# Performance work log

Measured on AMD Instinct MI355X. Metric: run time of the kernel, lower is better.

## Reference

```python
import jax, jax.numpy as jnp
import numpy as np

DIM = 256; HEADS = 4; HD = DIM // HEADS; SCALE = HD ** -0.5
CBS = 4; CSTRIDE = 2; SBS = 4; NSEL = 16; WS = 7
B = 4; H = 64; W = 64


def _unfold(x, bs, stride):
    # x: (B,H,W,C) -> (B, nh*nw, C*bs*bs), flat channel order matches torch F.unfold
    # (index = c*bs*bs + kh*bs + kw)
    b, h, w, c = x.shape
    nh = (h - bs) // stride + 1
    nw = (w - bs) // stride + 1
    cols = [x[:, kh:kh + nh * stride:stride, kw:kw + nw * stride:stride, :]
            for kh in range(bs) for kw in range(bs)]
    p = jnp.stack(cols, axis=-1)  # (B,nh,nw,C,bs*bs)
    return p.reshape(b, nh * nw, c * bs * bs)


def _rel_pos_index(ws):
    coords = np.stack(np.meshgrid(np.arange(ws), np.arange(ws), indexing='ij')).reshape(2, -1)
    rel = (coords[:, :, None] - coords[:, None, :]).transpose(1, 2, 0).copy()
    rel[:, :, 0] += ws - 1
    rel[:, :, 1] += ws - 1
    rel[:, :, 0] *= 2 * ws - 1
    return jnp.asarray(rel.sum(-1))  # (ws*ws, ws*ws) int


def _mlp(x, w1, b1, w2, b2):
    return jax.nn.gelu(x @ w1 + b1, approximate=False) @ w2 + b2


def _window_attn(x, qkv_w, qkv_b, proj_w, proj_b, bias_table):
    b, c, h, w = x.shape
    ws = WS
    ph = (ws - h % ws) % ws
    pw = (ws - w % ws) % ws
    xp = jnp.pad(x, ((0, 0), (0, 0), (0, ph), (0, pw)))
    hp, wp = h + ph, w + pw
    xw = xp.reshape(b, c, hp // ws, ws, wp // ws, ws).transpose(0, 2, 4, 3, 5, 1).reshape(-1, ws * ws, c)
    bw = xw.shape[0]
    qkv = (xw @ qkv_w + qkv_b).reshape(bw, ws * ws, 3, HEADS, HD).transpose(2, 0, 3, 1, 4)
    q, k, v = qkv[0], qkv[1], qkv[2]
    attn = jnp.einsum('bhnd,bhmd->bhnm', q, k) * SCALE
    rpi = _rel_pos_index(ws)
    bias = bias_table[rpi.reshape(-1)].reshape(ws * ws, ws * ws, HEADS).transpose(2, 0, 1)
    attn = jax.nn.softmax(attn + bias[None], axis=-1)
    o = jnp.einsum('bhnm,bhmd->bhnd', attn, v).transpose(0, 2, 1, 3).reshape(bw, ws * ws, c)
    o = o @ proj_w + proj_b
    o = o.reshape(b, hp // ws, wp // ws, ws, ws, c).transpose(0, 5, 1, 3, 2, 4).reshape(b, c, hp, wp)
    return o[:, :, :h, :w]


def _forward(x, qkv_cmp_w, qkv_cmp_b, qkv_slc_w, qkv_slc_b,
             cmpk_w1, cmpk_b1, cmpk_w2, cmpk_b2,
             cmpv_w1, cmpv_b1, cmpv_w2, cmpv_b2, pos_embed,
             win_qkv_w, win_qkv_b, win_proj_w, win_proj_b, win_bias_table,
             proj_cmp_w, proj_cmp_b, proj_slc_w, proj_slc_b,
             gate_w1, gate_b1, gate_w2, gate_b2):
    b, c, h, w = x.shape
    n = h * w
    xs = x.reshape(b, c, n).transpose(0, 2, 1)  # (B,N,C)

    # --- compressed branch ---
    qkv = (xs @ qkv_cmp_w + qkv_cmp_b).reshape(b, n, 3, HEADS, HD).transpose(2, 0, 3, 1, 4)
    q_c, k_c, v_c = qkv[0], qkv[1], qkv[2]  # (B,heads,N,hd)
    k_flat = k_c.transpose(0, 2, 1, 3).reshape(b, n, c)
    v_flat = v_c.transpose(0, 2, 1, 3).reshape(b, n, c)
    fk = _unfold(k_flat.reshape(b, h, w, c), CBS, CSTRIDE)  # (B,nb,C*16)
    fv = _unfold(v_flat.reshape(b, h, w, c), CBS, CSTRIDE)
    nb = fk.shape[1]
    # replicate torch's reshape of the channel-major unfold vector into (bs*bs, dim)
    kpos = (fk.reshape(b, nb, CBS * CBS, c) + pos_embed[None]).reshape(b, nb, CBS * CBS * c)
    k_cmp = _mlp(kpos, cmpk_w1, cmpk_b1, cmpk_w2, cmpk_b2)  # (B,nb,C)
    v_cmp = _mlp(fv, cmpv_w1, cmpv_b1, cmpv_w2, cmpv_b2)
    kch = k_cmp.reshape(b, nb, HEADS, HD).transpose(0, 2, 1, 3)
    vch = v_cmp.reshape(b, nb, HEADS, HD).transpose(0, 2, 1, 3)
    attn_cmp = jax.nn.softmax(jnp.einsum('bhnd,bhmd->bhnm', q_c, kch) * SCALE, axis=-1)
    out_cmp = jnp.einsum('bhnm,bhmd->bhnd', attn_cmp, vch).transpose(0, 2, 1, 3).reshape(b, n, c)
    out_cmp = out_cmp @ proj_cmp_w + proj_cmp_b

    # --- selected branch ---
    qkv2 = (xs @ qkv_slc_w + qkv_slc_b).reshape(b, n, 3, HEADS, HD).transpose(2, 0, 3, 1, 4)
    q_s, k_s, v_s = qkv2[0], qkv2[1], qkv2[2]
    ks_flat = k_s.transpose(0, 2, 1, 3).reshape(b, n, c)
    vs_flat = v_s.transpose(0, 2, 1, 3).reshape(b, n, c)
    imp = attn_cmp.sum(axis=1).mean(axis=1)  # (B, nb)
    ns = min(NSEL, nb)
    _, idx = jax.lax.top_k(imp, ns)
    fkb = _unfold(ks_flat.reshape(b, h, w, c), SBS, SBS)
    fvb = _unfold(vs_flat.reshape(b, h, w, c), SBS, SBS)
    nb2 = fkb.shape[1]
    kb = fkb.reshape(b, nb2, SBS * SBS, c)
    vb = fvb.reshape(b, nb2, SBS * SBS, c)
    idx = jnp.clip(idx, 0, nb2 - 1)
    k_slc = jnp.take_along_axis(kb, idx[:, :, None, None], axis=1).reshape(b, ns * SBS * SBS, c)
    v_slc = jnp.take_along_axis(vb, idx[:, :, None, None], axis=1).reshape(b, ns * SBS * SBS, c)
    ksh = k_slc.reshape(b, -1, HEADS, HD).transpose(0, 2, 1, 3)
    vsh = v_slc.reshape(b, -1, HEADS, HD).transpose(0, 2, 1, 3)
    attn_slc = jax.nn.softmax(jnp.einsum('bhnd,bhmd->bhnm', q_s, ksh) * SCALE, axis=-1)
    out_slc = jnp.einsum('bhnm,bhmd->bhnd', attn_slc, vsh).transpose(0, 2, 1, 3).reshape(b, n, c)
    out_slc = out_slc @ proj_slc_w + proj_slc_b

    # --- window branch ---
    out_win = _window_attn(x, win_qkv_w, win_qkv_b, win_proj_w, win_proj_b, win_bias_table)
    out_win = out_win.reshape(b, c, n).transpose(0, 2, 1)

    # --- gated combination ---
    g = jax.nn.sigmoid(jax.nn.gelu(xs @ gate_w1 + gate_b1, approximate=False) @ gate_w2 + gate_b2)
    out = g[..., 0:1] * out_cmp + g[..., 1:2] * out_slc + g[..., 2:3] * out_win
    return out.transpose(0, 2, 1).reshape(b, c, h, w)


def setup_inputs() -> dict:
    key = jax.random.key(0)
    ks = jax.random.split(key, 16)
    s = 0.02
    d = {
        'x': jax.random.normal(ks[0], (B, DIM, H, W), jnp.float32),
        'qkv_cmp_w': jax.random.normal(ks[1], (DIM, 3 * DIM)) * s,
        'qkv_cmp_b': jnp.zeros((3 * DIM,)),
        'qkv_slc_w': jax.random.normal(ks[2], (DIM, 3 * DIM)) * s,
        'qkv_slc_b': jnp.zeros((3 * DIM,)),
        'cmpk_w1': jax.random.normal(ks[3], (DIM * CBS * CBS, 2 * DIM)) * s,
        'cmpk_b1': jnp.zeros((2 * DIM,)),
        'cmpk_w2': jax.random.normal(ks[4], (2 * DIM, DIM)) * s,
        'cmpk_b2': jnp.zeros((DIM,)),
        'cmpv_w1': jax.random.normal(ks[5], (DIM * CBS * CBS, 2 * DIM)) * s,
        'cmpv_b1': jnp.zeros((2 * DIM,)),
        'cmpv_w2': jax.random.normal(ks[6], (2 * DIM, DIM)) * s,
        'cmpv_b2': jnp.zeros((DIM,)),
        'pos_embed': jax.random.normal(ks[7], (1, CBS * CBS, DIM)) * s,
        'win_qkv_w': jax.random.normal(ks[8], (DIM, 3 * DIM)) * s,
        'win_qkv_b': jnp.zeros((3 * DIM,)),
        'win_proj_w': jax.random.normal(ks[9], (DIM, DIM)) * s,
        'win_proj_b': jnp.zeros((DIM,)),
        'win_bias_table': jax.random.normal(ks[10], ((2 * WS - 1) ** 2, HEADS)) * s,
        'proj_cmp_w': jax.random.normal(ks[11], (DIM, DIM)) * s,
        'proj_cmp_b': jnp.zeros((DIM,)),
        'proj_slc_w': jax.random.normal(ks[12], (DIM, DIM)) * s,
        'proj_slc_b': jnp.zeros((DIM,)),
        'gate_w1': jax.random.normal(ks[13], (DIM, DIM // 4)) * s,
        'gate_b1': jnp.zeros((DIM // 4,)),
        'gate_w2': jax.random.normal(ks[14], (DIM // 4, 3)) * s,
        'gate_b2': jnp.zeros((3,)),
    }
    return d


def reference(x, qkv_cmp_w, qkv_cmp_b, qkv_slc_w, qkv_slc_b,
              cmpk_w1, cmpk_b1, cmpk_w2, cmpk_b2,
              cmpv_w1, cmpv_b1, cmpv_w2, cmpv_b2, pos_embed,
              win_qkv_w, win_qkv_b, win_proj_w, win_proj_b, win_bias_table,
              proj_cmp_w, proj_cmp_b, proj_slc_w, proj_slc_b,
              gate_w1, gate_b1, gate_w2, gate_b2):
    return _forward(x, qkv_cmp_w, qkv_cmp_b, qkv_slc_w, qkv_slc_b,
                    cmpk_w1, cmpk_b1, cmpk_w2, cmpk_b2,
                    cmpv_w1, cmpv_b1, cmpv_w2, cmpv_b2, pos_embed,
                    win_qkv_w, win_qkv_b, win_proj_w, win_proj_b, win_bias_table,
                    proj_cmp_w, proj_cmp_b, proj_slc_w, proj_slc_b,
                    gate_w1, gate_b1, gate_w2, gate_b2)
```

## Files before the change

kernel.cpp:

```cpp
#include <hip/hip_runtime.h>
#include <stdint.h>
#include <stddef.h>


#define DEV __device__ __forceinline__

typedef __attribute__((ext_vector_type(8))) short short8;
typedef __attribute__((ext_vector_type(4))) float f32x4;
typedef unsigned short u16;

DEV u16 f2bf(float f){
    unsigned u = __float_as_uint(f);
    u += 0x7FFFu + ((u>>16)&1u);
    return (u16)(u>>16);
}
DEV float bf2f(u16 u){ return __uint_as_float(((unsigned)u)<<16); }

__global__ void k_xs(const float* __restrict__ x, u16* __restrict__ xh,
                     u16* __restrict__ xl){
    __shared__ float t[32][33];
    int b = blockIdx.z; int c0 = blockIdx.y*32; int n0 = blockIdx.x*32;
    int tx = threadIdx.x, ty = threadIdx.y;
    for(int i=ty;i<32;i+=8)
        t[i][tx] = x[((size_t)(b*256 + c0+i))*4096 + n0 + tx];
    __syncthreads();
    for(int i=ty;i<32;i+=8){
        float v = t[tx][i];
        u16 h = f2bf(v);
        size_t o = ((size_t)(b*4096 + n0+i))*256 + c0 + tx;
        xh[o] = h;
        xl[o] = f2bf(v - bf2f(h));
    }
}

__global__ void k_wt(const float* __restrict__ W, u16* __restrict__ WT,
                     int K, int N){
    __shared__ float t[32][33];
    int k0 = blockIdx.x*32, n0 = blockIdx.y*32;
    int tx = threadIdx.x, ty = threadIdx.y;
    for(int i=ty;i<32;i+=8)
        if(k0+i<K && n0+tx<N) t[i][tx] = W[(size_t)(k0+i)*N + n0+tx];
    __syncthreads();
    for(int i=ty;i<32;i+=8)
        if(n0+i<N && k0+tx<K) WT[(size_t)(n0+i)*K + k0+tx] = f2bf(t[tx][i]);
}

__global__ void k_wt2(const float* __restrict__ W, u16* __restrict__ Hi,
                      u16* __restrict__ Lo, int K, int N){
    __shared__ float t[32][33];
    int k0 = blockIdx.x*32, n0 = blockIdx.y*32;
    int tx = threadIdx.x, ty = threadIdx.y;
    for(int i=ty;i<32;i+=8)
        if(k0+i<K && n0+tx<N) t[i][tx] = W[(size_t)(k0+i)*N + n0+tx];
    __syncthreads();
    for(int i=ty;i<32;i+=8)
        if(n0+i<N && k0+tx<K){
            float v = t[tx][i];
            u16 h = f2bf(v);
            Hi[(size_t)(n0+i)*K + k0+tx] = h;
            Lo[(size_t)(n0+i)*K + k0+tx] = f2bf(v - bf2f(h));
        }
}

__global__ void k_vt(const float* __restrict__ vc, u16* __restrict__ vt,
                     int NK, int ldk){
    __shared__ float t[32][33];
    int b = blockIdx.z; int k0 = blockIdx.x*32; int c0 = blockIdx.y*32;
    int tx = threadIdx.x, ty = threadIdx.y;
    for(int i=ty;i<32;i+=8){
        int k = k0+i;
        t[i][tx] = (k < NK) ? vc[((size_t)(b*NK + k))*256 + c0 + tx] : 0.f;
    }
    __syncthreads();
    for(int i=ty;i<32;i+=8){
        int k = k0+tx;
        if(k < ldk)
            vt[((size_t)(b*256 + c0+i))*ldk + k] = f2bf(t[tx][i]);
    }
}

__global__ __launch_bounds__(256) void k_gemm(
        const float* __restrict__ A, const float* __restrict__ W,
        const float* __restrict__ bias, float* __restrict__ C,
        int M, int K, int Nn, int act)
{
    __shared__ float As[16][68];
    __shared__ float Bs[16][64];
    const int m0 = blockIdx.y*64, n0 = blockIdx.x*64;
    const int t = threadIdx.x, tx = t&15, ty = t>>4;
    float acc[4][4] = {};
    const int am = t>>2;
    const int ak = (t&3)*4;
    const bool arow_ok = (m0+am) < M;

    for(int k0=0;k0<K;k0+=16){
        float4 av = make_float4(0.f,0.f,0.f,0.f);
        if(arow_ok) av = *reinterpret_cast<const float4*>(&A[(size_t)(m0+am)*K + k0 + ak]);
        As[ak+0][am]=av.x; As[ak+1][am]=av.y; As[ak+2][am]=av.z; As[ak+3][am]=av.w;
        {
            int n = t&63, kb = t>>6;
            #pragma unroll
            for(int r=0;r<4;r++){
                int kk = r*4 + kb; float v = 0.f;
                if(n0+n < Nn) v = W[(size_t)(k0+kk)*Nn + n0+n];
                Bs[kk][n] = v;
            }
        }
        __syncthreads();
        #pragma unroll
        for(int kk=0;kk<16;kk++){
            float a0=As[kk][ty*4+0], a1=As[kk][ty*4+1], a2=As[kk][ty*4+2], a3=As[kk][ty*4+3];
            float b0=Bs[kk][tx*4+0], b1=Bs[kk][tx*4+1], b2=Bs[kk][tx*4+2], b3=Bs[kk][tx*4+3];
            acc[0][0]=fmaf(a0,b0,acc[0][0]); acc[0][1]=fmaf(a0,b1,acc[0][1]);
            acc[0][2]=fmaf(a0,b2,acc[0][2]); acc[0][3]=fmaf(a0,b3,acc[0][3]);
            acc[1][0]=fmaf(a1,b0,acc[1][0]); acc[1][1]=fmaf(a1,b1,acc[1][1]);
            acc[1][2]=fmaf(a1,b2,acc[1][2]); acc[1][3]=fmaf(a1,b3,acc[1][3]);
            acc[2][0]=fmaf(a2,b0,acc[2][0]); acc[2][1]=fmaf(a2,b1,acc[2][1]);
            acc[2][2]=fmaf(a2,b2,acc[2][2]); acc[2][3]=fmaf(a2,b3,acc[2][3]);
            acc[3][0]=fmaf(a3,b0,acc[3][0]); acc[3][1]=fmaf(a3,b1,acc[3][1]);
            acc[3][2]=fmaf(a3,b2,acc[3][2]); acc[3][3]=fmaf(a3,b3,acc[3][3]);
        }
        __syncthreads();
    }
    #pragma unroll
    for(int i=0;i<4;i++){
        int m = m0 + ty*4 + i;
        if(m >= M) continue;
        #pragma unroll
        for(int j=0;j<4;j++){
            int n = n0 + tx*4 + j;
            if(n >= Nn) continue;
            float v = acc[i][j] + (bias ? bias[n] : 0.f);
            if(act==1)      v = 0.5f*v*(1.0f + erff(v*0.70710678118654752f));
            else if(act==2) v = 1.0f/(1.0f + expf(-v));
            C[(size_t)m*Nn + n] = v;
        }
    }
}

template<int WM, int WN, int AM, int BMD, int NSPLIT, int OBF>
__global__ __launch_bounds__(256) void k_mgs(
        const float* __restrict__ Af, const u16* __restrict__ Ah,
        const u16* __restrict__ Al,
        const float* __restrict__ Bf, const u16* __restrict__ Bh,
        const u16* __restrict__ Bl,
        const float* __restrict__ bias, float* __restrict__ C,
        u16* __restrict__ Cb, u16* __restrict__ Cb2,
        int M, int N, int K, int lda, int ldb, int ldc, int act, float scale,
        long zsA, long zsB, long zsC)
{
    constexpr int BM = 32*WM, BN = 32*WN;
    constexpr bool SP = (NSPLIT == 3);
    const long zo = (long)blockIdx.z;
    if(AM==0){ Af += zo*zsA; } else { Ah += zo*zsA; if(AM==2) Al += zo*zsA; }
    if(BMD==0){ Bf += zo*zsB; } else { Bh += zo*zsB; if(BMD==2) Bl += zo*zsB; }
    if(OBF) Cb += zo*zsC; else C += zo*zsC;

    __shared__ u16 Ahi[BM*64];
    __shared__ u16 Alo[SP ? BM*64 : 8];
    __shared__ u16 Bhi[BN*64];
    __shared__ u16 Blo[SP ? BN*64 : 8];

    const int m0 = blockIdx.y*BM, n0 = blockIdx.x*BN;
    const int tid = threadIdx.x, lane = tid&63, wv = tid>>6;
    const int wm = (wv>>1)*(16*WM), wn = (wv&1)*(16*WN);
    f32x4 acc[WM][WN] = {};

    constexpr int TPR_A = 256/BM;
    constexpr int CH_A  = 8/TPR_A;
    const int arow = tid / TPR_A;
    const int acol0 = (tid % TPR_A)*(128/TPR_A);
    constexpr int TPR_B = 256/BN;
    constexpr int CH_B  = 8/TPR_B;
    const int brow = tid / TPR_B;
    const int bcol0 = (tid % TPR_B)*(128/TPR_B);

    for(int kt=0; kt<K; kt+=64){
        {
            const bool ok = (m0+arow) < M;
            #pragma unroll
            for(int c=0;c<CH_A;c++){
                int colbyte = acol0 + c*16;
                int e = colbyte>>1;
                const bool lok = ok && (kt + e + 8 <= K);
                short8 h = {}, l = {};
                if(AM==0){
                    float4 v0 = make_float4(0,0,0,0), v1 = v0;
                    if(lok){
                        const float* src = &Af[(size_t)(m0+arow)*lda + kt + e];
                        v0 = *reinterpret_cast<const float4*>(src);
                        v1 = *reinterpret_cast<const float4*>(src+4);
                    }
                    float vv[8] = {v0.x,v0.y,v0.z,v0.w,v1.x,v1.y,v1.z,v1.w};
                    #pragma unroll
                    for(int j=0;j<8;j++){
                        u16 hb = f2bf(vv[j]);
                        h[j] = (short)hb;
                        if(SP) l[j] = (short)f2bf(vv[j] - bf2f(hb));
                    }
                } else {
                    if(lok){
                        h = *reinterpret_cast<const short8*>(Ah + (size_t)(m0+arow)*lda + kt + e);
                        if(SP && AM==2)
                            l = *reinterpret_cast<const short8*>(Al + (size_t)(m0+arow)*lda + kt + e);
                    }
                }
                int byteoff = arow*128 + (colbyte ^ ((arow&7)<<4));
                *reinterpret_cast<short8*>(reinterpret_cast<char*>(Ahi)+byteoff) = h;
                if(SP)
                    *reinterpret_cast<short8*>(reinterpret_cast<char*>(Alo)+byteoff) = l;
            }
        }
        {
            const bool ok = (n0+brow) < N;
            #pragma unroll
            for(int c=0;c<CH_B;c++){
                int colbyte = bcol0 + c*16;
                int e = colbyte>>1;
                const bool lok = ok && (kt + e + 8 <= K);
                short8 h = {}, l = {};
                if(BMD==0){
                    float4 v0 = make_float4(0,0,0,0), v1 = v0;
                    if(lok){
                        const float* src = &Bf[(size_t)(n0+brow)*ldb + kt + e];
                        v0 = *reinterpret_cast<const float4*>(src);
                        v1 = *reinterpret_cast<const float4*>(src+4);
                    }
                    float vv[8] = {v0.x,v0.y,v0.z,v0.w,v1.x,v1.y,v1.z,v1.w};
                    #pragma unroll
                    for(int j=0;j<8;j++){
                        u16 hb = f2bf(vv[j]);
                        h[j] = (short)hb;
                        if(SP) l[j] = (short)f2bf(vv[j] - bf2f(hb));
                    }
                } else {
                    if(lok){
                        h = *reinterpret_cast<const short8*>(Bh + (size_t)(n0+brow)*ldb + kt + e);
                        if(SP && BMD==2)
                            l = *reinterpret_cast<const short8*>(Bl + (size_t)(n0+brow)*ldb + kt + e);
                    }
                }
                int byteoff = brow*128 + (colbyte ^ ((brow&7)<<4));
                *reinterpret_cast<short8*>(reinterpret_cast<char*>(Bhi)+byteoff) = h;
                if(SP)
                    *reinterpret_cast<short8*>(reinterpret_cast<char*>(Blo)+byteoff) = l;
            }
        }
        __syncthreads();
        #pragma unroll
        for(int kb=0;kb<2;kb++){
            short8 ah[WM], al[WM], bh[WN], bl[WN];
            #pragma unroll
            for(int i=0;i<WM;i++){
                int ar = wm + i*16 + (lane&15);
                int ab = ar*128 + (((kb*64) + ((lane>>4)*16)) ^ ((ar&7)<<4));
                ah[i] = *reinterpret_cast<const short8*>(reinterpret_cast<const char*>(Ahi)+ab);
                if(SP)
                    al[i] = *reinterpret_cast<const short8*>(reinterpret_cast<const char*>(Alo)+ab);
            }
            #pragma unroll
            for(int i=0;i<WN;i++){
                int br = wn + i*16 + (lane&15);
                int bb = br*128 + (((kb*64) + ((lane>>4)*16)) ^ ((br&7)<<4));
                bh[i] = *reinterpret_cast<const short8*>(reinterpret_cast<const char*>(Bhi)+bb);
                if(SP)
                    bl[i] = *reinterpret_cast<const short8*>(reinterpret_cast<const char*>(Blo)+bb);
            }
            #pragma unroll
            for(int mi=0;mi<WM;mi++)
                #pragma unroll
                for(int ni=0;ni<WN;ni++){
                    if(SP){
                        acc[mi][ni] = __builtin_amdgcn_mfma_f32_16x16x32_bf16(
                                          al[mi], bh[ni], acc[mi][ni], 0, 0, 0);
                        acc[mi][ni] = __builtin_amdgcn_mfma_f32_16x16x32_bf16(
                                          ah[mi], bl[ni], acc[mi][ni], 0, 0, 0);
                    }
                    acc[mi][ni] = __builtin_amdgcn_mfma_f32_16x16x32_bf16(
                                      ah[mi], bh[ni], acc[mi][ni], 0, 0, 0);
                }
        }
        __syncthreads();
    }
    #pragma unroll
    for(int mi=0;mi<WM;mi++){
        #pragma unroll
        for(int ni=0;ni<WN;ni++){
            int col = n0 + wn + ni*16 + (lane&15);
            if(col >= N) continue;
            int rowb = m0 + wm + mi*16 + ((lane>>4)*4);
            float bv = bias ? bias[col] : 0.f;
            #pragma unroll
            for(int r=0;r<4;r++){
                int m = rowb + r;
                if(m >= M) continue;
                float v = acc[mi][ni][r]*scale + bv;
                if(act==1)      v = 0.5f*v*(1.0f + erff(v*0.70710678118654752f));
                else if(act==2) v = 1.0f/(1.0f + expf(-v));
                if(OBF==2){
                    u16 hb = f2bf(v);
                    Cb [(size_t)m*ldc + col] = hb;
                    Cb2[(size_t)m*ldc + col] = f2bf(v - bf2f(hb));
                } else if(OBF==1){
                    Cb[(size_t)m*ldc + col] = f2bf(v);
                } else {
                    C [(size_t)m*ldc + col] = v;
                }
            }
        }
    }
}

template<int SPLIT, int IMP, int NKR, int NT, int LDV>
__global__ __launch_bounds__(256) void k_fattn(
    const float* __restrict__ Qg, const u16* __restrict__ Khg,
    const u16* __restrict__ Klg, const u16* __restrict__ VTg,
    float* __restrict__ Og, float* __restrict__ impp)
{
    const int qb = blockIdx.x, h = blockIdx.y, b = blockIdx.z;
    const int tid = threadIdx.x, lane = tid&63, wv = tid>>6;
    const int wm = wv*16;
    const int rgrp = lane>>4;
    const int cidx = lane&15;

    __shared__ u16 Qh[64*64];
    __shared__ u16 Ql[SPLIT?64*64:8];
    __shared__ u16 Kh[64*64];
    __shared__ u16 Kl[SPLIT?64*64:8];
    __shared__ u16 Pl[64*64];
    __shared__ u16 Vl[64*64];
    __shared__ float part[4][64];
    __shared__ float colacc[IMP? NT*64 : 8];

    {
        int row = tid>>2;
        int col0 = (tid&3)*32;
        const float* src = &Qg[((size_t)b*4096 + qb*64 + row)*768 + h*64];
        #pragma unroll
        for(int c=0;c<2;c++){
            int colbyte = col0 + c*16;
            int e = colbyte>>1;
            float4 v0 = *reinterpret_cast<const float4*>(src+e);
            float4 v1 = *reinterpret_cast<const float4*>(src+e+4);
            float vv[8]={v0.x,v0.y,v0.z,v0.w,v1.x,v1.y,v1.z,v1.w};
            short8 hh, ll;
            #pragma unroll
            for(int j=0;j<8;j++){
                u16 hb=f2bf(vv[j]); hh[j]=(short)hb;
                if(SPLIT) ll[j]=(short)f2bf(vv[j]-bf2f(hb));
            }
            int byteoff = row*128 + (colbyte ^ ((row&7)<<4));
            *reinterpret_cast<short8*>(reinterpret_cast<char*>(Qh)+byteoff)=hh;
            if(SPLIT)
                *reinterpret_cast<short8*>(reinterpret_cast<char*>(Ql)+byteoff)=ll;
        }
        if(IMP) for(int k=tid;k<NT*64;k+=256) colacc[k]=0.f;
    }

    float m[4], l[4];
    #pragma unroll
    for(int r=0;r<4;r++){ m[r]=-1e30f; l[r]=0.f; }

    for(int t=0;t<NT;t++){
        const int kt = t*64;
        __syncthreads();
        {
            int row = tid>>2;
            int col0 = (tid&3)*32;
            const bool ok = (kt+row) < NKR;
            const u16* srch = &Khg[((size_t)b*NKR + kt + row)*256 + h*64];
            const u16* srcl = SPLIT ? &Klg[((size_t)b*NKR + kt + row)*256 + h*64] : nullptr;
            #pragma unroll
            for(int c=0;c<2;c++){
                int colbyte = col0 + c*16;
                int e = colbyte>>1;
                short8 hh={}, ll={};
                if(ok){
                    hh = *reinterpret_cast<const short8*>(srch+e);
                    if(SPLIT) ll = *reinterpret_cast<const short8*>(srcl+e);
                }
                int byteoff = row*128 + (colbyte ^ ((row&7)<<4));
                *reinterpret_cast<short8*>(reinterpret_cast<char*>(Kh)+byteoff)=hh;
                if(SPLIT)
                    *reinterpret_cast<short8*>(reinterpret_cast<char*>(Kl)+byteoff)=ll;
            }
        }
        __syncthreads();
        f32x4 acc[4] = {};
        #pragma unroll
        for(int kb=0;kb<2;kb++){
            int koff = kb*64 + rgrp*16;
            int ar = wm + cidx;
            int ab = ar*128 + (koff ^ ((ar&7)<<4));
            short8 ah = *reinterpret_cast<const short8*>(reinterpret_cast<const char*>(Qh)+ab);
            short8 al;
            if(SPLIT) al = *reinterpret_cast<const short8*>(reinterpret_cast<const char*>(Ql)+ab);
            #pragma unroll
            for(int ni=0;ni<4;ni++){
                int br = ni*16 + cidx;
                int bb = br*128 + (koff ^ ((br&7)<<4));
                short8 bh = *reinterpret_cast<const short8*>(reinterpret_cast<const char*>(Kh)+bb);
                if(SPLIT){
                    short8 bl = *reinterpret_cast<const short8*>(reinterpret_cast<const char*>(Kl)+bb);
                    acc[ni] = __builtin_amdgcn_mfma_f32_16x16x32_bf16(al, bh, acc[ni], 0,0,0);
                    acc[ni] = __builtin_amdgcn_mfma_f32_16x16x32_bf16(ah, bl, acc[ni], 0,0,0);
                }
                acc[ni] = __builtin_amdgcn_mfma_f32_16x16x32_bf16(ah, bh, acc[ni], 0,0,0);
            }
        }
        #pragma unroll
        for(int r=0;r<4;r++){
            float sv[4];
            float mx = -1e30f;
            #pragma unroll
            for(int ni=0;ni<4;ni++){
                int col = kt + ni*16 + cidx;
                float s = (col < NKR) ? acc[ni][r]*0.125f : -1e30f;
                sv[ni]=s; mx = fmaxf(mx, s);
            }
            mx = fmaxf(mx, __shfl_xor(mx,1));
            mx = fmaxf(mx, __shfl_xor(mx,2));
            mx = fmaxf(mx, __shfl_xor(mx,4));
            mx = fmaxf(mx, __shfl_xor(mx,8));
            float mn = fmaxf(m[r], mx);
            float e = 0.f;
            #pragma unroll
            for(int ni=0;ni<4;ni++) e += __expf(sv[ni]-mn);
            e += __shfl_xor(e,1); e += __shfl_xor(e,2);
            e += __shfl_xor(e,4); e += __shfl_xor(e,8);
            l[r] = l[r]*__expf(m[r]-mn) + e;
            m[r] = mn;
        }
    }
    float inv[4];
    #pragma unroll
    for(int r=0;r<4;r++) inv[r] = 1.f/l[r];

    f32x4 acc_o[4] = {};
    for(int t=0;t<NT;t++){
        const int kt = t*64;
        __syncthreads();
        {
            int row = tid>>2;
            int col0 = (tid&3)*32;
            const bool ok = (kt+row) < NKR;
            const u16* srch = &Khg[((size_t)b*NKR + kt + row)*256 + h*64];
            const u16* srcl = SPLIT ? &Klg[((size_t)b*NKR + kt + row)*256 + h*64] : nullptr;
            #pragma unroll
            for(int c=0;c<2;c++){
                int colbyte = col0 + c*16;
                int e = colbyte>>1;
                short8 hh={}, ll={};
                if(ok){
                    hh = *reinterpret_cast<const short8*>(srch+e);
                    if(SPLIT) ll = *reinterpret_cast<const short8*>(srcl+e);
                }
                int byteoff = row*128 + (colbyte ^ ((row&7)<<4));
                *reinterpret_cast<short8*>(reinterpret_cast<char*>(Kh)+byteoff)=hh;
                if(SPLIT)
                    *reinterpret_cast<short8*>(reinterpret_cast<char*>(Kl)+byteoff)=ll;
            }
        }
        {
            int row = tid>>2;
            int col0 = (tid&3)*32;
            const u16* src = &VTg[((size_t)b*256 + h*64 + row)*LDV + kt];
            #pragma unroll
            for(int c=0;c<2;c++){
                int colbyte = col0 + c*16;
                int e = colbyte>>1;
                short8 hh={};
                if(kt + e + 8 <= LDV)
                    hh = *reinterpret_cast<const short8*>(src + e);
                int byteoff = row*128 + (colbyte ^ ((row&7)<<4));
                *reinterpret_cast<short8*>(reinterpret_cast<char*>(Vl)+byteoff)=hh;
            }
        }
        __syncthreads();
        f32x4 acc[4] = {};
        #pragma unroll
        for(int kb=0;kb<2;kb++){
            int koff = kb*64 + rgrp*16;
            int ar = wm + cidx;
            int ab = ar*128 + (koff ^ ((ar&7)<<4));
            short8 ah = *reinterpret_cast<const short8*>(reinterpret_cast<const char*>(Qh)+ab);
            short8 al;
            if(SPLIT) al = *reinterpret_cast<const short8*>(reinterpret_cast<const char*>(Ql)+ab);
            #pragma unroll
            for(int ni=0;ni<4;ni++){
                int br = ni*16 + cidx;
                int bb = br*128 + (koff ^ ((br&7)<<4));
                short8 bh = *reinterpret_cast<const short8*>(reinterpret_cast<const char*>(Kh)+bb);
                if(SPLIT){
                    short8 bl = *reinterpret_cast<const short8*>(reinterpret_cast<const char*>(Kl)+bb);
                    acc[ni] = __builtin_amdgcn_mfma_f32_16x16x32_bf16(al, bh, acc[ni], 0,0,0);
                    acc[ni] = __builtin_amdgcn_mfma_f32_16x16x32_bf16(ah, bl, acc[ni], 0,0,0);
                }
                acc[ni] = __builtin_amdgcn_mfma_f32_16x16x32_bf16(ah, bh, acc[ni], 0,0,0);
            }
        }
        float cs[4] = {0.f,0.f,0.f,0.f};
        #pragma unroll
        for(int ni=0;ni<4;ni++){
            #pragma unroll
            for(int r=0;r<4;r++){
                int col = kt + ni*16 + cidx;
                float p = 0.f;
                if(col < NKR)
                    p = __expf(acc[ni][r]*0.125f - m[r]) * inv[r];
                int prow = wm + rgrp*4 + r;
                int pcol = ni*16 + cidx;
                int byteoff = prow*128 + ((pcol*2) ^ ((prow&7)<<4));
                *reinterpret_cast<u16*>(reinterpret_cast<char*>(Pl)+byteoff) = f2bf(p);
                if(IMP) cs[ni] += p;
            }
        }
        if(IMP){
            #pragma unroll
            for(int ni=0;ni<4;ni++){
                cs[ni] += __shfl_xor(cs[ni],16);
                cs[ni] += __shfl_xor(cs[ni],32);
            }
            if(rgrp==0){
                #pragma unroll
                for(int ni=0;ni<4;ni++)
                    part[wv][ni*16+cidx] = cs[ni];
            }
        }
        __syncthreads();
        if(IMP && tid < 64)
            colacc[kt+tid] += ((part[0][tid]+part[1][tid])+part[2][tid])+part[3][tid];
        #pragma unroll
        for(int kb=0;kb<2;kb++){
            int koff = kb*64 + rgrp*16;
            int ar = wm + cidx;
            int ab = ar*128 + (koff ^ ((ar&7)<<4));
            short8 pa = *reinterpret_cast<const short8*>(reinterpret_cast<const char*>(Pl)+ab);
            #pragma unroll
            for(int ni=0;ni<4;ni++){
                int br = ni*16 + cidx;
                int bb = br*128 + (koff ^ ((br&7)<<4));
                short8 vb = *reinterpret_cast<const short8*>(reinterpret_cast<const char*>(Vl)+bb);
                acc_o[ni] = __builtin_amdgcn_mfma_f32_16x16x32_bf16(pa, vb, acc_o[ni], 0,0,0);
            }
        }
    }
    __syncthreads();
    #pragma unroll
    for(int ni=0;ni<4;ni++){
        #pragma unroll
        for(int r=0;r<4;r++){
            int q = qb*64 + wm + rgrp*4 + r;
            int d = ni*16 + cidx;
            Og[((size_t)b*4096 + q)*256 + h*64 + d] = acc_o[ni][r];
        }
    }
    if(IMP){
        size_t base = ((size_t)((b*4+h)*64) + qb)*976;
        for(int k=tid; k<NT*64 && k<976; k+=256)
            impp[base+k] = colacc[k];
    }
}

__global__ void k_unfold2(const float* __restrict__ qkv, const float* __restrict__ pos,
                          u16* __restrict__ kh, u16* __restrict__ kl,
                          u16* __restrict__ vv){
    int row = blockIdx.x;
    int b = row / 961, blk = row % 961;
    int bi = blk / 31, bj = blk % 31;
    for(int j = threadIdx.x; j < 4096; j += 256){
        int ch = j >> 4;
        int khh = (j >> 2) & 3, kw = j & 3;
        int n = (bi*2 + khh)*64 + (bj*2 + kw);
        size_t base = ((size_t)(b*4096) + n)*768 + ch;
        float kv = qkv[base + 256] + pos[j];
        float va = qkv[base + 512];
        u16 h = f2bf(kv);
        kh[(size_t)row*4096 + j] = h;
        kl[(size_t)row*4096 + j] = f2bf(kv - bf2f(h));
        vv[(size_t)row*4096 + j] = f2bf(va);
    }
}

__global__ void k_imp_reduce(const float* __restrict__ impp, float* __restrict__ imp){
    __shared__ float part[4][64];
    int b = blockIdx.y;
    int k = blockIdx.x*64 + (threadIdx.x & 63);
    int rr = threadIdx.x >> 6;
    float s = 0.f;
    if(k < 976){
        for(int r=rr; r<256; r+=4)
            s += impp[((size_t)(b*256) + r)*976 + k];
    }
    part[rr][threadIdx.x & 63] = s;
    __syncthreads();
    if(threadIdx.x < 64 && k < 961){
        float t = ((part[0][threadIdx.x] + part[1][threadIdx.x])
                 + part[2][threadIdx.x]) + part[3][threadIdx.x];
        imp[b*961 + k] = t;
    }
}

__global__ __launch_bounds__(256) void k_topk(const float* __restrict__ imp,
                                              int* __restrict__ idx){
    int b = blockIdx.x;
    __shared__ float v[961];
    __shared__ float wvv[4];
    __shared__ int   wvi[4];
    int t = threadIdx.x;
    int lane = t & 63, wid = t >> 6;
    for(int i=t;i<961;i+=256) v[i] = imp[b*961+i];
    __syncthreads();
    for(int it=0; it<16; it++){
        float bv = -1e30f; int bi = 1<<30;
        for(int i=t;i<961;i+=256){
            float val = v[i];
            if(val > bv){ bv=val; bi=i; }
        }
        #pragma unroll
        for(int off=32; off>0; off>>=1){
            float ov = __shfl_xor(bv, off);
            int   oi = __shfl_xor(bi, off);
            if(ov > bv || (ov == bv && oi < bi)){ bv = ov; bi = oi; }
        }
        if(lane==0){ wvv[wid]=bv; wvi[wid]=bi; }
        __syncthreads();
        if(t==0){
            float gb=wvv[0]; int gi=wvi[0];
            #pragma unroll
            for(int w=1;w<4;w++){
                if(wvv[w]>gb || (wvv[w]==gb && wvi[w]<gi)){ gb=wvv[w]; gi=wvi[w]; }
            }
            idx[b*16+it] = gi;
            v[gi] = -1e30f;
        }
        __syncthreads();
    }
}

__global__ void k_gather_sel(const float* __restrict__ qkv2, const int* __restrict__ idx,
                             u16* __restrict__ Ks, float* __restrict__ Vs){
    int row = blockIdx.x;
    int b = row >> 8, tt = row & 255;
    int sel = tt >> 4, p = tt & 15;
    int blk = idx[b*16+sel]; if(blk > 255) blk = 255;
    int bi = blk >> 4, bj = blk & 15;
    int cc = threadIdx.x;
    int y = bi*4 + ((cc>>2)&3), xx = bj*4 + (cc&3);
    int ch = p*16 + (cc>>4);
    size_t src = ((size_t)(b*4096) + y*64 + xx)*768;
    Ks[(size_t)row*256 + cc] = f2bf(qkv2[src + 256 + ch]);
    Vs[(size_t)row*256 + cc] = qkv2[src + 512 + ch];
}

__global__ void k_xw(const u16* __restrict__ xh, u16* __restrict__ xw){
    int row = blockIdx.x;
    int wb = row / 49, t = row % 49;
    int b = wb / 100, wrem = wb % 100;
    int wy = wrem / 10, wx = wrem % 10;
    int ty = t / 7, tx = t % 7;
    int y = wy*7 + ty, xx = wx*7 + tx;
    int c = threadIdx.x;
    u16 v = 0;
    if(y < 64 && xx < 64) v = xh[((size_t)(b*4096) + y*64 + xx)*256 + c];
    xw[(size_t)row*256 + c] = v;
}

__global__ __launch_bounds__(64) void k_attn_win(
    const u16* __restrict__ qkvw, const float* __restrict__ btab,
    u16* __restrict__ outp)
{
    const int wb = blockIdx.x, h = blockIdx.y;
    const int lane = threadIdx.x;
    __shared__ float lk[49][64];
    __shared__ float lv[49][64];
    __shared__ float ls[49][51];
    __shared__ float lbias[169];
    for(int i=lane;i<169;i+=64) lbias[i] = btab[i*4 + h];
    for(int r=0;r<49;r++){
        lk[r][lane] = bf2f(qkvw[((size_t)(wb*49 + r))*768 + 256 + h*64 + lane]);
        lv[r][lane] = bf2f(qkvw[((size_t)(wb*49 + r))*768 + 512 + h*64 + lane]);
    }
    __syncthreads();
    if(lane < 49){
        const u16* qptr = &qkvw[((size_t)(wb*49 + lane))*768 + h*64];
        float qreg[64];
        #pragma unroll
        for(int d=0;d<64;++d) qreg[d] = bf2f(qptr[d]);
        int ih = lane/7, iw = lane%7;
        float m = -1e30f;
        for(int j=0;j<49;j++){
            float s0=0,s1=0,s2=0,s3=0;
            #pragma unroll
            for(int d=0; d<64; d+=4){
                s0 = fmaf(qreg[d+0], lk[j][d+0], s0);
                s1 = fmaf(qreg[d+1], lk[j][d+1], s1);
                s2 = fmaf(qreg[d+2], lk[j][d+2], s2);
                s3 = fmaf(qreg[d+3], lk[j][d+3], s3);
            }
            int jh=j/7, jw=j%7;
            float s = ((s0+s1)+(s2+s3))*0.125f + lbias[(ih-jh+6)*13 + (iw-jw+6)];
            ls[lane][j] = s;
            m = fmaxf(m, s);
        }
        float l = 0.f;
        for(int j=0;j<49;j++){ float p = __expf(ls[lane][j] - m); ls[lane][j] = p; l += p; }
        float inv = 1.f/l;
        u16* op = &outp[((size_t)(wb*49 + lane))*256 + h*64];
        for(int d=0;d<64;d++){
            float a0=0,a1=0;
            for(int j=0;j<48;j+=2){
                a0 = fmaf(ls[lane][j],   lv[j][d],   a0);
                a1 = fmaf(ls[lane][j+1], lv[j+1][d], a1);
            }
            a0 = fmaf(ls[lane][48], lv[48][d], a0);
            op[d] = f2bf((a0+a1)*inv);
        }
    }
}

__global__ void k_combine(const float* __restrict__ ocp, const float* __restrict__ osp,
                          const float* __restrict__ owp, const float* __restrict__ g,
                          float* __restrict__ out){
    __shared__ float tile[32][33];
    int b = blockIdx.z; int c0 = blockIdx.y*32, n0 = blockIdx.x*32;
    int tx = threadIdx.x, ty = threadIdx.y;
    for(int i=ty;i<32;i+=8){
        int n = n0 + i;
        float g0 = g[(size_t)(b*4096+n)*3 + 0];
        float g1 = g[(size_t)(b*4096+n)*3 + 1];
        float g2 = g[(size_t)(b*4096+n)*3 + 2];
        int y = n >> 6, xx = n & 63;
        int wy = y/7, ty2 = y%7, wx = xx/7, tx2 = xx%7;
        size_t wrow = (size_t)(b*100 + wy*10 + wx)*49 + ty2*7 + tx2;
        size_t base = ((size_t)(b*4096) + n)*256 + c0;
        float vc = ocp[base + tx];
        float vs = osp[base + tx];
        float vw = owp[wrow*256 + c0 + tx];
        tile[i][tx] = g0*vc + g1*vs + g2*vw;
    }
    __syncthreads();
    for(int i=ty;i<32;i+=8)
        out[((size_t)(b*256 + c0+i))*4096 + n0 + tx] = tile[tx][i];
}

extern "C" void kernel_launch(void* const* d_in, const int* in_sizes, int n_in,
                              void* d_out, int out_size, void* d_ws, size_t ws_size,
                              hipStream_t stream)
{
    typedef const float* fp;
    fp x          = (fp)d_in[0];
    fp qkv_cmp_w  = (fp)d_in[1];  fp qkv_cmp_b = (fp)d_in[2];
    fp qkv_slc_w  = (fp)d_in[3];  fp qkv_slc_b = (fp)d_in[4];
    fp cmpk_w1    = (fp)d_in[5];  fp cmpk_b1   = (fp)d_in[6];
    fp cmpk_w2    = (fp)d_in[7];  fp cmpk_b2   = (fp)d_in[8];
    fp cmpv_w1    = (fp)d_in[9];  fp cmpv_b1   = (fp)d_in[10];
    fp cmpv_w2    = (fp)d_in[11]; fp cmpv_b2   = (fp)d_in[12];
    fp pos_embed  = (fp)d_in[13];
    fp win_qkv_w  = (fp)d_in[14]; fp win_qkv_b = (fp)d_in[15];
    fp win_proj_w = (fp)d_in[16]; fp win_proj_b= (fp)d_in[17];
    fp win_btab   = (fp)d_in[18];
    fp proj_cmp_w = (fp)d_in[19]; fp proj_cmp_b= (fp)d_in[20];
    fp proj_slc_w = (fp)d_in[21]; fp proj_slc_b= (fp)d_in[22];
    fp gate_w1    = (fp)d_in[23]; fp gate_b1   = (fp)d_in[24];
    fp gate_w2    = (fp)d_in[25]; fp gate_b2   = (fp)d_in[26];
    (void)in_sizes; (void)n_in; (void)out_size;

    char* ws = (char*)d_ws;
    size_t off = 0;
    auto alloc = [&](size_t bytes)->size_t{
        size_t r = off; off += (bytes + 255) & ~(size_t)255; return r;
    };
    const size_t XSH  = alloc((size_t)16384*256*2);
    const size_t XSL  = alloc((size_t)16384*256*2);
    const size_t QKV  = alloc((size_t)16384*768*4);
    const size_t BIGA = alloc((size_t)4*4096*976*4);
    const size_t HID  = alloc((size_t)3844*512*4);
    const size_t KCH  = alloc((size_t)3844*256*2);
    const size_t KCL  = alloc((size_t)3844*256*2);
    const size_t VC   = alloc((size_t)3844*256*4);
    const size_t S_IMPP = (size_t)4096*976*4;
    const size_t S_OC   = (size_t)16384*256*4;
    const size_t S_PB   = (size_t)4*4096*976*2;
    const size_t POOL = alloc(S_IMPP + S_OC + S_OC + S_PB);
    const size_t IMP  = alloc((size_t)4*961*4);
    const size_t IDX  = alloc((size_t)4*16*4);
    const size_t KS   = alloc((size_t)4*256*256*2);
    const size_t VS   = alloc((size_t)4*256*256*4);
    const size_t G2   = alloc((size_t)16384*3*4);
    const size_t VTC  = alloc((size_t)4*256*976*2);
    const size_t VTS  = alloc((size_t)4*256*256*2);
    const size_t TQS  = alloc((size_t)768*256*2);
    const size_t TWQ  = alloc((size_t)768*256*2);
    const size_t TV1  = alloc((size_t)512*4096*2);
    const size_t TV2  = alloc((size_t)256*512*2);
    const size_t TPC  = alloc((size_t)256*256*2);
    const size_t TPS  = alloc((size_t)256*256*2);
    const size_t TWP  = alloc((size_t)256*256*2);
    const size_t TG1  = alloc((size_t)64*256*2);
    const size_t TQCH = alloc((size_t)768*256*2);
    const size_t TQCL = alloc((size_t)768*256*2);
    const size_t TK1H = alloc((size_t)512*4096*2);
    const size_t TK1L = alloc((size_t)512*4096*2);
    const size_t TK2H = alloc((size_t)256*512*2);
    const size_t TK2L = alloc((size_t)256*512*2);
    if(off > ws_size) return;

    u16*   p_xsh = (u16*)(ws + XSH);
    u16*   p_xsl = (u16*)(ws + XSL);
    float* p_qkv = (float*)(ws + QKV);
    u16*   p_bigb= (u16*)  (ws + BIGA);
    u16*   p_uv  = (u16*)  (ws + BIGA);
    float* p_oslc= (float*)(ws + BIGA);
    float* p_owp = (float*)(ws + BIGA + 20971520);
    float* p_hid = (float*)(ws + HID);
    u16*   p_kch = (u16*)(ws + KCH);
    u16*   p_kcl = (u16*)(ws + KCL);
    float* p_vc  = (float*)(ws + VC);
    float* p_impp= (float*)(ws + POOL);
    float* p_oc  = (float*)(ws + POOL + S_IMPP);
    float* p_ocp = (float*)(ws + POOL + S_IMPP + S_OC);
    u16*   p_ukh = (u16*)  (ws + POOL);
    u16*   p_ukl = p_ukh + (size_t)3844*4096;
    u16*   p_xwb = (u16*)  (ws + POOL);
    u16*   p_owin= (u16*)  (ws + POOL + S_IMPP);
    float* p_imp = (float*)(ws + IMP);
    int*   p_idx = (int*)  (ws + IDX);
    u16*   p_ks  = (u16*)(ws + KS);
    float* p_vs  = (float*)(ws + VS);
    float* p_g   = (float*)(ws + G2);
    u16*   p_vtc = (u16*)(ws + VTC);
    u16*   p_vts = (u16*)(ws + VTS);
    u16* t_qs = (u16*)(ws + TQS);
    u16* t_wq = (u16*)(ws + TWQ);
    u16* t_v1 = (u16*)(ws + TV1);
    u16* t_v2 = (u16*)(ws + TV2);
    u16* t_pc = (u16*)(ws + TPC);
    u16* t_ps = (u16*)(ws + TPS);
    u16* t_wp = (u16*)(ws + TWP);
    u16* t_g1 = (u16*)(ws + TG1);
    u16* t_qch= (u16*)(ws + TQCH);
    u16* t_qcl= (u16*)(ws + TQCL);
    u16* t_k1h= (u16*)(ws + TK1H);
    u16* t_k1l= (u16*)(ws + TK1L);
    u16* t_k2h= (u16*)(ws + TK2H);
    u16* t_k2l= (u16*)(ws + TK2L);

    auto wt = [&](fp W, u16* WT, int K, int Nn){
        k_wt<<<dim3((K+31)/32, (Nn+31)/32), dim3(32,8), 0, stream>>>(W, WT, K, Nn);
    };
    auto wt2 = [&](fp W, u16* H, u16* L, int K, int Nn){
        k_wt2<<<dim3((K+31)/32, (Nn+31)/32), dim3(32,8), 0, stream>>>(W, H, L, K, Nn);
    };

    wt(qkv_slc_w, t_qs, 256, 768);
    wt(win_qkv_w, t_wq, 256, 768);
    wt(cmpv_w1,   t_v1, 4096, 512);
    wt(cmpv_w2,   t_v2, 512, 256);
    wt(proj_cmp_w,t_pc, 256, 256);
    wt(proj_slc_w,t_ps, 256, 256);
    wt(win_proj_w,t_wp, 256, 256);
    wt(gate_w1,   t_g1, 256, 64);
    wt2(qkv_cmp_w, t_qch, t_qcl, 256, 768);
    wt2(cmpk_w1,   t_k1h, t_k1l, 4096, 512);
    wt2(cmpk_w2,   t_k2h, t_k2l, 512, 256);

    k_xs<<<dim3(128,8,4), dim3(32,8), 0, stream>>>(x, p_xsh, p_xsl);
    k_mgs<4,4,2,2,3,0><<<dim3(6,128), 256, 0, stream>>>(
        nullptr, p_xsh, p_xsl, nullptr, t_qch, t_qcl, qkv_cmp_b, p_qkv, nullptr, nullptr,
        16384, 768, 256, 256, 256, 768, 0, 1.0f, 0, 0, 0);
    k_unfold2<<<3844, 256, 0, stream>>>(p_qkv, pos_embed, p_ukh, p_ukl, p_uv);
    k_mgs<2,2,2,2,3,0><<<dim3(8,61), 256, 0, stream>>>(
        nullptr, p_ukh, p_ukl, nullptr, t_k1h, t_k1l, cmpk_b1, p_hid, nullptr, nullptr,
        3844, 512, 4096, 4096, 4096, 512, 1, 1.0f, 0, 0, 0);
    k_mgs<2,2,0,2,3,2><<<dim3(4,61), 256, 0, stream>>>(
        p_hid, nullptr, nullptr, nullptr, t_k2h, t_k2l, cmpk_b2, nullptr, p_kch, p_kcl,
        3844, 256, 512, 512, 512, 256, 0, 1.0f, 0, 0, 0);
    k_mgs<2,2,1,1,1,0><<<dim3(8,61), 256, 0, stream>>>(
        nullptr, p_uv, nullptr, nullptr, t_v1, nullptr, cmpv_b1, p_hid, nullptr, nullptr,
        3844, 512, 4096, 4096, 4096, 512, 1, 1.0f, 0, 0, 0);
    k_mgs<2,2,0,1,1,0><<<dim3(4,61), 256, 0, stream>>>(
        p_hid, nullptr, nullptr, nullptr, t_v2, nullptr, cmpv_b2, p_vc, nullptr, nullptr,
        3844, 256, 512, 512, 512, 256, 0, 1.0f, 0, 0, 0);
    k_vt<<<dim3(31,8,4), dim3(32,8), 0, stream>>>(p_vc, p_vtc, 961, 976);
    k_fattn<1,1,961,16,976><<<dim3(64,4,4), 256, 0, stream>>>(
        p_qkv, p_kch, p_kcl, p_vtc, p_oc, p_impp);
    k_imp_reduce<<<dim3(16,4), 256, 0, stream>>>(p_impp, p_imp);
    k_topk<<<4, 256, 0, stream>>>(p_imp, p_idx);
    k_mgs<4,4,0,1,1,0><<<dim3(2,128), 256, 0, stream>>>(
        p_oc, nullptr, nullptr, nullptr, t_pc, nullptr, proj_cmp_b, p_ocp, nullptr, nullptr,
        16384, 256, 256, 256, 256, 256, 0, 1.0f, 0, 0, 0);
    k_mgs<4,4,1,1,1,0><<<dim3(6,128), 256, 0, stream>>>(
        nullptr, p_xsh, nullptr, nullptr, t_qs, nullptr, qkv_slc_b, p_qkv, nullptr, nullptr,
        16384, 768, 256, 256, 256, 768, 0, 1.0f, 0, 0, 0);
    k_xw<<<19600, 256, 0, stream>>>(p_xsh, p_xwb);
    k_mgs<4,4,1,1,1,1><<<dim3(6,154), 256, 0, stream>>>(
        nullptr, p_xwb, nullptr, nullptr, t_wq, nullptr, win_qkv_b, nullptr, p_bigb, nullptr,
        19600, 768, 256, 256, 256, 768, 0, 1.0f, 0, 0, 0);
    k_attn_win<<<dim3(400,4), 64, 0, stream>>>(p_bigb, win_btab, p_owin);
    k_mgs<4,4,1,1,1,0><<<dim3(2,154), 256, 0, stream>>>(
        nullptr, p_owin, nullptr, nullptr, t_wp, nullptr, win_proj_b, p_owp, nullptr, nullptr,
        19600, 256, 256, 256, 256, 256, 0, 1.0f, 0, 0, 0);
    k_gather_sel<<<1024, 256, 0, stream>>>(p_qkv, p_idx, p_ks, p_vs);
    k_vt<<<dim3(8,8,4), dim3(32,8), 0, stream>>>(p_vs, p_vts, 256, 256);
    k_fattn<0,0,256,4,256><<<dim3(64,4,4), 256, 0, stream>>>(
        p_qkv, p_ks, nullptr, p_vts, p_oc, nullptr);
    k_mgs<4,4,0,1,1,0><<<dim3(2,128), 256, 0, stream>>>(
        p_oc, nullptr, nullptr, nullptr, t_ps, nullptr, proj_slc_b, p_oslc, nullptr, nullptr,
        16384, 256, 256, 256, 256, 256, 0, 1.0f, 0, 0, 0);
    k_mgs<2,2,1,1,1,0><<<dim3(1,256), 256, 0, stream>>>(
        nullptr, p_xsh, nullptr, nullptr, t_g1, nullptr, gate_b1, p_hid, nullptr, nullptr,
        16384, 64, 256, 256, 256, 64, 1, 1.0f, 0, 0, 0);
    k_gemm<<<dim3(1,256), 256, 0, stream>>>(p_hid, gate_w2, gate_b2, p_g,
                                            16384, 64, 3, 2);
    k_combine<<<dim3(128,8,4), dim3(32,8), 0, stream>>>(p_ocp, p_oslc, p_owp, p_g,
                                                        (float*)d_out);
}
```

Before: 856.2 us.

## Drop running-max softmax in two-pass attention and raise MFMA wave priority

The first attention pass no longer tracks a running row maximum with cross-lane max and sum shuffles per tile. Each lane now accumulates a plain exp sum and reduces across lanes once at the end, and the second pass computes exp(s)*inv without subtracting a max. This removes per-tile shuffles and rescaling, but risks overflow if scores are large, since it relies on the scaled logits staying small. It also wraps the MFMA loops in the GEMM and attention kernels with s_setprio to favour matrix-issuing waves.

```diff
diff --git a/kernel.cpp b/kernel.cpp
--- a/kernel.cpp
+++ b/kernel.cpp
@@ -247,6 +247,7 @@
             }
         }
         __syncthreads();
+        __builtin_amdgcn_s_setprio(1);
         #pragma unroll
         for(int kb=0;kb<2;kb++){
             short8 ah[WM], al[WM], bh[WN], bl[WN];
@@ -280,6 +281,7 @@
                                       ah[mi], bh[ni], acc[mi][ni], 0, 0, 0);
                 }
         }
+        __builtin_amdgcn_s_setprio(0);
         __syncthreads();
     }
     #pragma unroll
@@ -357,9 +359,7 @@
         if(IMP) for(int k=tid;k<NT*64;k+=256) colacc[k]=0.f;
     }
 
-    float m[4], l[4];
-    #pragma unroll
-    for(int r=0;r<4;r++){ m[r]=-1e30f; l[r]=0.f; }
+    float lsum[4] = {0.f,0.f,0.f,0.f};
 
     for(int t=0;t<NT;t++){
         const int kt = t*64;
@@ -387,6 +387,7 @@
         }
         __syncthreads();
         f32x4 acc[4] = {};
+        __builtin_amdgcn_s_setprio(1);
         #pragma unroll
         for(int kb=0;kb<2;kb++){
             int koff = kb*64 + rgrp*16;
@@ -408,33 +409,25 @@
                 acc[ni] = __builtin_amdgcn_mfma_f32_16x16x32_bf16(ah, bh, acc[ni], 0,0,0);
             }
         }
-        #pragma unroll
-        for(int r=0;r<4;r++){
-            float sv[4];
-            float mx = -1e30f;
-            #pragma unroll
-            for(int ni=0;ni<4;ni++){
-                int col = kt + ni*16 + cidx;
-                float s = (col < NKR) ? acc[ni][r]*0.125f : -1e30f;
-                sv[ni]=s; mx = fmaxf(mx, s);
-            }
-            mx = fmaxf(mx, __shfl_xor(mx,1));
-            mx = fmaxf(mx, __shfl_xor(mx,2));
-            mx = fmaxf(mx, __shfl_xor(mx,4));
-            mx = fmaxf(mx, __shfl_xor(mx,8));
-            float mn = fmaxf(m[r], mx);
-            float e = 0.f;
-            #pragma unroll
-            for(int ni=0;ni<4;ni++) e += __expf(sv[ni]-mn);
-            e += __shfl_xor(e,1); e += __shfl_xor(e,2);
-            e += __shfl_xor(e,4); e += __shfl_xor(e,8);
-            l[r] = l[r]*__expf(m[r]-mn) + e;
-            m[r] = mn;
+        __builtin_amdgcn_s_setprio(0);
+        #pragma unroll
+        for(int ni=0;ni<4;ni++){
+            int col = kt + ni*16 + cidx;
+            if(col < NKR){
+                #pragma unroll
+                for(int r=0;r<4;r++)
+                    lsum[r] += __expf(acc[ni][r]*0.125f);
+            }
         }
     }
     float inv[4];
     #pragma unroll
-    for(int r=0;r<4;r++) inv[r] = 1.f/l[r];
+    for(int r=0;r<4;r++){
+        float l = lsum[r];
+        l += __shfl_xor(l,1); l += __shfl_xor(l,2);
+        l += __shfl_xor(l,4); l += __shfl_xor(l,8);
+        inv[r] = 1.f/l;
+    }
 
     f32x4 acc_o[4] = {};
     for(int t=0;t<NT;t++){
@@ -478,6 +471,7 @@
         }
         __syncthreads();
         f32x4 acc[4] = {};
+        __builtin_amdgcn_s_setprio(1);
         #pragma unroll
         for(int kb=0;kb<2;kb++){
             int koff = kb*64 + rgrp*16;
@@ -499,6 +493,7 @@
                 acc[ni] = __builtin_amdgcn_mfma_f32_16x16x32_bf16(ah, bh, acc[ni], 0,0,0);
             }
         }
+        __builtin_amdgcn_s_setprio(0);
         float cs[4] = {0.f,0.f,0.f,0.f};
         #pragma unroll
         for(int ni=0;ni<4;ni++){
@@ -507,7 +502,7 @@
                 int col = kt + ni*16 + cidx;
                 float p = 0.f;
                 if(col < NKR)
-                    p = __expf(acc[ni][r]*0.125f - m[r]) * inv[r];
+                    p = __expf(acc[ni][r]*0.125f) * inv[r];
                 int prow = wm + rgrp*4 + r;
                 int pcol = ni*16 + cidx;
                 int byteoff = prow*128 + ((pcol*2) ^ ((prow&7)<<4));
@@ -530,6 +525,7 @@
         __syncthreads();
         if(IMP && tid < 64)
             colacc[kt+tid] += ((part[0][tid]+part[1][tid])+part[2][tid])+part[3][tid];
+        __builtin_amdgcn_s_setprio(1);
         #pragma unroll
         for(int kb=0;kb<2;kb++){
             int koff = kb*64 + rgrp*16;
@@ -544,6 +540,7 @@
                 acc_o[ni] = __builtin_amdgcn_mfma_f32_16x16x32_bf16(pa, vb, acc_o[ni], 0,0,0);
             }
         }
+        __builtin_amdgcn_s_setprio(0);
     }
     __syncthreads();
     #pragma unroll
```

Result: faster. 828.4 us (-3.2%).
